# Kernel optimization log

Hardware: AMD Instinct MI355X
Metric: run time of the kernel (lower is better)

## Reference

```python
import jax, jax.numpy as jnp
import numpy as np

B, C, H, W = 8, 128, 256, 256
D = 64            # embed_dim
S = 32            # max_segments


def setup_inputs() -> dict:
    key = jax.random.key(0)
    ks = jax.random.split(key, 8)
    return {
        "segment_labels": jax.random.randint(ks[0], (B, 1, H, W), 0, S, dtype=jnp.int32),
        "features": jax.random.normal(ks[1], (B, C, H, W), jnp.float32),
        # 1x1 conv stack feat_proj: Conv2d(C->D), ReLU, Conv2d(D->D)
        "conv1_w": jax.random.normal(ks[2], (D, C), jnp.float32) * 0.05,
        "conv1_b": jnp.zeros((D,), jnp.float32),
        "conv2_w": jax.random.normal(ks[3], (D, D), jnp.float32) * 0.1,
        "conv2_b": jnp.zeros((D,), jnp.float32),
        # nn.Embedding(max_segments + 1, embed_dim)
        "embed_table": jax.random.normal(ks[4], (S + 1, D), jnp.float32) * 0.02,
        # nn.Linear(2*D, D): y = x @ W.T + b, W is (out, in)
        "out_w": jax.random.normal(ks[5], (D, 2 * D), jnp.float32) * 0.05,
        "out_b": jnp.zeros((D,), jnp.float32),
    }


def reference(segment_labels, features, conv1_w, conv1_b, conv2_w, conv2_b,
              embed_table, out_w, out_b):
    Bb, Cc, Hh, Ww = features.shape
    P = Hh * Ww
    Smax = embed_table.shape[0] - 1  # max_segments

    # feat_proj: two 1x1 convs == per-pixel GEMMs
    x = features.reshape(Bb, Cc, P)                                   # (B,C,P)
    h1 = jnp.maximum(jnp.einsum('oc,bcp->bpo', conv1_w, x) + conv1_b, 0.0)  # (B,P,D)
    feat = jnp.einsum('od,bpd->bpo', conv2_w, h1) + conv2_b           # (B,P,D)

    # Per-(batch, segment-id) masked mean via a single segment-sum pass.
    labels = segment_labels[:, 0].reshape(Bb, P)                       # (B,P) in [0,S)
    ids = (labels + Smax * jnp.arange(Bb, dtype=labels.dtype)[:, None]).reshape(-1)
    sums = jax.ops.segment_sum(feat.reshape(Bb * P, -1), ids,
                               num_segments=Bb * Smax).reshape(Bb, Smax, -1)
    counts = jax.ops.segment_sum(jnp.ones((Bb * P,), feat.dtype), ids,
                                 num_segments=Bb * Smax).reshape(Bb, Smax)
    pooled = sums / jnp.maximum(counts, 1.0)[..., None]                # (B,S,D) (zeros where absent)

    # type embedding for seg_id s (already in [0,S), clamp is a no-op but faithful)
    type_emb = embed_table[jnp.clip(jnp.arange(Smax), 0, Smax)]        # (S,D)
    combined = jnp.concatenate(
        [pooled, jnp.broadcast_to(type_emb, (Bb, Smax, type_emb.shape[-1]))], axis=-1)
    combined = jnp.einsum('oe,bse->bso', out_w, combined) + out_b      # (B,S,D)

    # torch.unique returns sorted present labels; compact present segments to the
    # front (rank order), pad rest with zeros.
    present = counts > 0                                               # (B,S)
    rank = jnp.cumsum(present.astype(jnp.int32), axis=1) - 1
    dst = jnp.where(present, rank, Smax)                               # Smax = dropped slot
    bidx = jnp.broadcast_to(jnp.arange(Bb)[:, None], (Bb, Smax))
    out = jnp.zeros_like(combined)
    out = out.at[bidx, dst].set(combined, mode='drop')
    return out
```

## Files before the change

### kernel.cpp

```cpp
#include <hip/hip_runtime.h>


#define B_ 8
#define C_ 128
#define P_ 65536
#define D_ 64
#define S_ 32
#define PXT 256
#define ROWPAD 260

typedef short bf16x8 __attribute__((ext_vector_type(8)));
typedef float f32x4  __attribute__((ext_vector_type(4)));

__device__ __forceinline__ short f2bf(float f) {
  union { float f; unsigned u; } v; v.f = f;
  unsigned r = v.u + 0x7fffu + ((v.u >> 16) & 1u);
  return (short)(r >> 16);
}

__global__ __launch_bounds__(256) void w1_to_bf16(const float* __restrict__ w1,
                                                  short* __restrict__ wbf) {
  int i = blockIdx.x * 256 + threadIdx.x;
  if (i < C_ * D_) wbf[i] = f2bf(w1[i]);
}

__device__ __forceinline__ void gload16(const float* g, const float* l) {
  __builtin_amdgcn_global_load_lds(
      (const __attribute__((address_space(1))) float*)g,
      (__attribute__((address_space(3))) float*)l, 16, 0, 0);
}

__global__ __launch_bounds__(256, 2) void proj_mfma(
    const int* __restrict__ labels, const float* __restrict__ feat,
    const short* __restrict__ wbf, const float* __restrict__ b1,
    float* __restrict__ gsum, int* __restrict__ gcnt)
{
  __shared__ __align__(16) float ring[4][16 * ROWPAD];
  __shared__ float s_acc[S_][68];
  __shared__ int   s_cnt[S_];

  const int tid  = threadIdx.x;
  const int wave = tid >> 6, l = tid & 63, m = l & 15, g = l >> 4;
  const int b    = blockIdx.y;
  const int px0  = blockIdx.x * PXT;

  for (int i = tid; i < S_ * 68; i += 256) ((float*)s_acc)[i] = 0.f;
  if (tid < S_) s_cnt[tid] = 0;

  bf16x8 bfr[4][4];
  #pragma unroll
  for (int nt = 0; nt < 4; ++nt)
    #pragma unroll
    for (int u = 0; u < 4; ++u)
      bfr[nt][u] = *(const bf16x8*)&wbf[(nt * 16 + m) * C_ + u * 32 + g * 8];
  float b1v[4];
  #pragma unroll
  for (int nt = 0; nt < 4; ++nt) b1v[nt] = b1[nt * 16 + m];

  const float* xb = feat + (size_t)b * C_ * P_ + px0;

#define STAGE(c_) do {                                                        \
    _Pragma("unroll") for (int i = 0; i < 4; ++i)                             \
      gload16(xb + (size_t)((c_) * 16 + wave * 4 + i) * P_ + l * 4,           \
              &ring[(c_) & 3][(wave * 4 + i) * ROWPAD]);                      \
  } while (0)

#define WAITV(n_) do {                                                        \
    asm volatile("s_waitcnt vmcnt(" #n_ ")" ::: "memory");                    \
    __builtin_amdgcn_sched_barrier(0);                                        \
  } while (0)

#define PAIR(u_) do {                                                         \
    _Pragma("unroll") for (int v = 0; v < 4; ++v) {                           \
      const int px = wave * 64 + v * 16 + m;                                  \
      const float* sl = &ring[(2 * (u_) + (g >> 1)) & 3]                      \
                             [((g & 1) * 8) * ROWPAD + px];                   \
      bf16x8 af;                                                              \
      _Pragma("unroll") for (int j = 0; j < 8; ++j)                           \
        af[j] = f2bf(sl[j * ROWPAD]);                                         \
      _Pragma("unroll") for (int nt = 0; nt < 4; ++nt)                        \
        acc[v][nt] = __builtin_amdgcn_mfma_f32_16x16x32_bf16(                 \
            af, bfr[nt][u_], acc[v][nt], 0, 0, 0);                            \
    }                                                                         \
  } while (0)

  STAGE(0); STAGE(1); STAGE(2); STAGE(3);

  f32x4 acc[4][4];
  #pragma unroll
  for (int v = 0; v < 4; ++v)
    #pragma unroll
    for (int nt = 0; nt < 4; ++nt) acc[v][nt] = (f32x4){0.f, 0.f, 0.f, 0.f};

  WAITV(8);
  __builtin_amdgcn_s_barrier();
  PAIR(0);
  __builtin_amdgcn_sched_barrier(0);
  __builtin_amdgcn_s_barrier();
  STAGE(4); STAGE(5);
  WAITV(8);
  __builtin_amdgcn_s_barrier();
  PAIR(1);
  __builtin_amdgcn_sched_barrier(0);
  __builtin_amdgcn_s_barrier();
  STAGE(6); STAGE(7);
  WAITV(8);
  __builtin_amdgcn_s_barrier();
  PAIR(2);
  __builtin_amdgcn_sched_barrier(0);
  WAITV(0);
  __builtin_amdgcn_s_barrier();
  PAIR(3);
  __builtin_amdgcn_sched_barrier(0);

#undef STAGE
#undef WAITV
#undef PAIR

  const int* lb = labels + (size_t)b * P_ + px0 + wave * 64;
  #pragma unroll
  for (int v = 0; v < 4; ++v) {
    const int4 lv = *(const int4*)&lb[v * 16 + g * 4];
    #pragma unroll
    for (int nt = 0; nt < 4; ++nt) {
      #pragma unroll
      for (int r = 0; r < 4; ++r) {
        const int lab = ((r & 2) ? ((r & 1) ? lv.w : lv.z)
                                 : ((r & 1) ? lv.y : lv.x)) & (S_ - 1);
        atomicAdd(&s_acc[lab][nt * 16 + m],
                  fmaxf(acc[v][nt][r] + b1v[nt], 0.f));
      }
    }
    if (m < 4) {
      const int lab = ((m & 2) ? ((m & 1) ? lv.w : lv.z)
                               : ((m & 1) ? lv.y : lv.x)) & (S_ - 1);
      atomicAdd(&s_cnt[lab], 1);
    }
  }

  __syncthreads();
  for (int i = tid; i < S_ * D_; i += 256)
    atomicAdd(&gsum[(size_t)b * S_ * D_ + i], s_acc[i >> 6][i & 63]);
  if (tid < S_) atomicAdd(&gcnt[b * S_ + tid], s_cnt[tid]);
}

__global__ __launch_bounds__(64) void seg_finalize2(
    const float* __restrict__ gsum, const int* __restrict__ gcnt,
    const float* __restrict__ w2, const float* __restrict__ b2,
    const float* __restrict__ emb, const float* __restrict__ wo,
    const float* __restrict__ bo, float* __restrict__ out)
{
  const int s = blockIdx.x, b = blockIdx.y, o = threadIdx.x;
  const int co = (o < S_) ? gcnt[b * S_ + o] : 0;
  const unsigned long long mask = __ballot(co > 0);
  const int cnt = gcnt[b * S_ + s];
  if (cnt <= 0) return;
  const int rank = __popcll(mask & ((1ull << s) - 1ull));

  __shared__ float s_mean[D_], s_pool[D_];
  s_mean[o] = gsum[((size_t)b * S_ + s) * D_ + o] * (1.f / (float)cnt);
  __syncthreads();
  float pooled = b2[o];
  #pragma unroll
  for (int d = 0; d < D_; ++d) pooled += w2[o * D_ + d] * s_mean[d];
  s_pool[o] = pooled;
  __syncthreads();
  float r = bo[o];
  #pragma unroll
  for (int e = 0; e < D_; ++e) r += wo[o * 2 * D_ + e] * s_pool[e];
  #pragma unroll
  for (int e = 0; e < D_; ++e) r += wo[o * 2 * D_ + D_ + e] * emb[s * D_ + e];
  out[((size_t)b * S_ + rank) * D_ + o] = r;
}

extern "C" void kernel_launch(void* const* d_in, const int* in_sizes, int n_in,
                              void* d_out, int out_size, void* d_ws, size_t ws_size,
                              hipStream_t stream) {
  const int*   labels = (const int*)  d_in[0];
  const float* feat   = (const float*)d_in[1];
  const float* w1     = (const float*)d_in[2];
  const float* b1     = (const float*)d_in[3];
  const float* w2     = (const float*)d_in[4];
  const float* b2     = (const float*)d_in[5];
  const float* emb    = (const float*)d_in[6];
  const float* wo     = (const float*)d_in[7];
  const float* bo     = (const float*)d_in[8];
  float* out = (float*)d_out;

  char* w = (char*)d_ws;
  float* gsum = (float*)w;   w += (size_t)B_ * S_ * D_ * 4;
  int*   gcnt = (int*)w;     w += (size_t)B_ * S_ * 4;
  short* wbf  = (short*)w;

  hipMemsetAsync(d_ws, 0, (size_t)B_ * S_ * D_ * 4 + (size_t)B_ * S_ * 4, stream);
  hipMemsetAsync(d_out, 0, (size_t)out_size * sizeof(float), stream);

  w1_to_bf16<<<(C_ * D_ + 255) / 256, 256, 0, stream>>>(w1, wbf);

  dim3 grid(P_ / PXT, B_);
  proj_mfma<<<grid, 256, 0, stream>>>(labels, feat, wbf, b1, gsum, gcnt);
  seg_finalize2<<<dim3(S_, B_), 64, 0, stream>>>(gsum, gcnt, w2, b2, emb, wo, bo, out);
}
```

Measured before the change: 233.0 us.

## Retile projection kernel to 1024-pixel blocks with 32x32 MFMA and LDS weights

Rewrites the projection kernel to use 512-thread blocks covering 1024 pixels each, with a 16-step ring pipeline over 8-channel slabs. It switches from 16x16x32 to 32x32x16 bf16 MFMA, stages the bf16 weights through padded LDS instead of per-thread registers, and remaps block ids so consecutive blocks land on different batches/XCDs. Fewer blocks mean fewer global atomic flushes of segment sums, but the larger LDS footprint and block size may reduce occupancy and latency hiding.

```diff
diff --git a/kernel.cpp b/kernel.cpp
--- a/kernel.cpp
+++ b/kernel.cpp
@@ -6,11 +6,12 @@
 #define P_ 65536
 #define D_ 64
 #define S_ 32
-#define PXT 256
-#define ROWPAD 260
+#define PXB 1024
+#define RP  1024
+#define WP  136
 
 typedef short bf16x8 __attribute__((ext_vector_type(8)));
-typedef float f32x4  __attribute__((ext_vector_type(4)));
+typedef float f32x16 __attribute__((ext_vector_type(16)));
 
 __device__ __forceinline__ short f2bf(float f) {
   union { float f; unsigned u; } v; v.f = f;
@@ -30,39 +31,37 @@
       (__attribute__((address_space(3))) float*)l, 16, 0, 0);
 }
 
-__global__ __launch_bounds__(256, 2) void proj_mfma(
+__global__ __launch_bounds__(512, 2) void proj_mfma(
     const int* __restrict__ labels, const float* __restrict__ feat,
     const short* __restrict__ wbf, const float* __restrict__ b1,
     float* __restrict__ gsum, int* __restrict__ gcnt)
 {
-  __shared__ __align__(16) float ring[4][16 * ROWPAD];
+  __shared__ __align__(16) float ring[4][8 * RP];
+  __shared__ __align__(16) short wlds[D_ * WP];
   __shared__ float s_acc[S_][68];
   __shared__ int   s_cnt[S_];
 
-  const int tid  = threadIdx.x;
-  const int wave = tid >> 6, l = tid & 63, m = l & 15, g = l >> 4;
-  const int b    = blockIdx.y;
-  const int px0  = blockIdx.x * PXT;
+  const int tid = threadIdx.x;
+  const int w = tid >> 6, l = tid & 63, n = l & 31, h = l >> 5;
+  const int bid = blockIdx.x;
+  const int wk  = (bid & 7) * 64 + (bid >> 3);
+  const int b   = wk >> 6;
+  const int px0 = (wk & 63) * PXB;
 
-  for (int i = tid; i < S_ * 68; i += 256) ((float*)s_acc)[i] = 0.f;
+  for (int i = tid; i < S_ * 68; i += 512) ((float*)s_acc)[i] = 0.f;
   if (tid < S_) s_cnt[tid] = 0;
-
-  bf16x8 bfr[4][4];
-  #pragma unroll
-  for (int nt = 0; nt < 4; ++nt)
-    #pragma unroll
-    for (int u = 0; u < 4; ++u)
-      bfr[nt][u] = *(const bf16x8*)&wbf[(nt * 16 + m) * C_ + u * 32 + g * 8];
-  float b1v[4];
-  #pragma unroll
-  for (int nt = 0; nt < 4; ++nt) b1v[nt] = b1[nt * 16 + m];
+  {
+    const int d = tid >> 3, c0 = (tid & 7) * 16;
+    *(bf16x8*)&wlds[d * WP + c0]     = *(const bf16x8*)&wbf[d * C_ + c0];
+    *(bf16x8*)&wlds[d * WP + c0 + 8] = *(const bf16x8*)&wbf[d * C_ + c0 + 8];
+  }
 
   const float* xb = feat + (size_t)b * C_ * P_ + px0;
 
-#define STAGE(c_) do {                                                        \
+#define STAGE(ci) do {                                                        \
     _Pragma("unroll") for (int i = 0; i < 4; ++i)                             \
-      gload16(xb + (size_t)((c_) * 16 + wave * 4 + i) * P_ + l * 4,           \
-              &ring[(c_) & 3][(wave * 4 + i) * ROWPAD]);                      \
+      gload16(xb + (size_t)((ci) * 8 + w) * P_ + i * 256 + l * 4,             \
+              &ring[(ci) & 3][w * RP + i * 256]);                             \
   } while (0)
 
 #define WAITV(n_) do {                                                        \
@@ -70,76 +69,67 @@
     __builtin_amdgcn_sched_barrier(0);                                        \
   } while (0)
 
-#define PAIR(u_) do {                                                         \
-    _Pragma("unroll") for (int v = 0; v < 4; ++v) {                           \
-      const int px = wave * 64 + v * 16 + m;                                  \
-      const float* sl = &ring[(2 * (u_) + (g >> 1)) & 3]                      \
-                             [((g & 1) * 8) * ROWPAD + px];                   \
-      bf16x8 af;                                                              \
-      _Pragma("unroll") for (int j = 0; j < 8; ++j)                           \
-        af[j] = f2bf(sl[j * ROWPAD]);                                         \
-      _Pragma("unroll") for (int nt = 0; nt < 4; ++nt)                        \
-        acc[v][nt] = __builtin_amdgcn_mfma_f32_16x16x32_bf16(                 \
-            af, bfr[nt][u_], acc[v][nt], 0, 0, 0);                            \
-    }                                                                         \
-  } while (0)
+  STAGE(0); STAGE(1); STAGE(2); STAGE(3);
+  asm volatile("s_waitcnt lgkmcnt(0)" ::: "memory");
+  __builtin_amdgcn_sched_barrier(0);
 
-  STAGE(0); STAGE(1); STAGE(2); STAGE(3);
-
-  f32x4 acc[4][4];
+  f32x16 acc[4][2];
   #pragma unroll
   for (int v = 0; v < 4; ++v)
     #pragma unroll
-    for (int nt = 0; nt < 4; ++nt) acc[v][nt] = (f32x4){0.f, 0.f, 0.f, 0.f};
+    for (int nt = 0; nt < 2; ++nt)
+      #pragma unroll
+      for (int e = 0; e < 16; ++e) acc[v][nt][e] = 0.f;
 
-  WAITV(8);
-  __builtin_amdgcn_s_barrier();
-  PAIR(0);
-  __builtin_amdgcn_sched_barrier(0);
-  __builtin_amdgcn_s_barrier();
-  STAGE(4); STAGE(5);
-  WAITV(8);
-  __builtin_amdgcn_s_barrier();
-  PAIR(1);
-  __builtin_amdgcn_sched_barrier(0);
-  __builtin_amdgcn_s_barrier();
-  STAGE(6); STAGE(7);
-  WAITV(8);
-  __builtin_amdgcn_s_barrier();
-  PAIR(2);
-  __builtin_amdgcn_sched_barrier(0);
-  WAITV(0);
-  __builtin_amdgcn_s_barrier();
-  PAIR(3);
-  __builtin_amdgcn_sched_barrier(0);
+  #pragma unroll
+  for (int ks = 0; ks < 8; ++ks) {
+    if (ks < 7) { WAITV(8); } else { WAITV(0); }
+    __builtin_amdgcn_s_barrier();
+    __builtin_amdgcn_sched_barrier(0);
 
+    const bf16x8 bw0 = *(const bf16x8*)&wlds[n * WP + ks * 16 + h * 8];
+    const bf16x8 bw1 = *(const bf16x8*)&wlds[(32 + n) * WP + ks * 16 + h * 8];
+    const float* rs = &ring[(2 * ks + h) & 3][0];
+    #pragma unroll
+    for (int v = 0; v < 4; ++v) {
+      bf16x8 af;
+      #pragma unroll
+      for (int j = 0; j < 8; ++j)
+        af[j] = f2bf(rs[j * RP + (w * 4 + v) * 32 + n]);
+      acc[v][0] = __builtin_amdgcn_mfma_f32_32x32x16_bf16(af, bw0, acc[v][0], 0, 0, 0);
+      acc[v][1] = __builtin_amdgcn_mfma_f32_32x32x16_bf16(af, bw1, acc[v][1], 0, 0, 0);
+    }
+    __builtin_amdgcn_sched_barrier(0);
+    __builtin_amdgcn_s_barrier();
+    __builtin_amdgcn_sched_barrier(0);
+    if (ks < 6) { STAGE(2 * ks + 4); STAGE(2 * ks + 5); }
+  }
 #undef STAGE
 #undef WAITV
-#undef PAIR
 
-  const int* lb = labels + (size_t)b * P_ + px0 + wave * 64;
+  const float b1v0 = b1[n];
+  const float b1v1 = b1[32 + n];
+  const int* lb = labels + (size_t)b * P_ + px0;
   #pragma unroll
   for (int v = 0; v < 4; ++v) {
-    const int4 lv = *(const int4*)&lb[v * 16 + g * 4];
+    const int tb = (w * 4 + v) * 32;
     #pragma unroll
-    for (int nt = 0; nt < 4; ++nt) {
+    for (int q = 0; q < 4; ++q) {
+      const int4 lv = *(const int4*)&lb[tb + q * 8 + h * 4];
       #pragma unroll
-      for (int r = 0; r < 4; ++r) {
-        const int lab = ((r & 2) ? ((r & 1) ? lv.w : lv.z)
-                                 : ((r & 1) ? lv.y : lv.x)) & (S_ - 1);
-        atomicAdd(&s_acc[lab][nt * 16 + m],
-                  fmaxf(acc[v][nt][r] + b1v[nt], 0.f));
+      for (int r2 = 0; r2 < 4; ++r2) {
+        const int lab = ((r2 & 2) ? ((r2 & 1) ? lv.w : lv.z)
+                                  : ((r2 & 1) ? lv.y : lv.x)) & (S_ - 1);
+        const int rg = q * 4 + r2;
+        atomicAdd(&s_acc[lab][n],      fmaxf(acc[v][0][rg] + b1v0, 0.f));
+        atomicAdd(&s_acc[lab][32 + n], fmaxf(acc[v][1][rg] + b1v1, 0.f));
+        if (n == 0) atomicAdd(&s_cnt[lab], 1);
       }
-    }
-    if (m < 4) {
-      const int lab = ((m & 2) ? ((m & 1) ? lv.w : lv.z)
-                               : ((m & 1) ? lv.y : lv.x)) & (S_ - 1);
-      atomicAdd(&s_cnt[lab], 1);
     }
   }
 
   __syncthreads();
-  for (int i = tid; i < S_ * D_; i += 256)
+  for (int i = tid; i < S_ * D_; i += 512)
     atomicAdd(&gsum[(size_t)b * S_ * D_ + i], s_acc[i >> 6][i & 63]);
   if (tid < S_) atomicAdd(&gcnt[b * S_ + tid], s_cnt[tid]);
 }
@@ -197,7 +187,6 @@
 
   w1_to_bf16<<<(C_ * D_ + 255) / 256, 256, 0, stream>>>(w1, wbf);
 
-  dim3 grid(P_ / PXT, B_);
-  proj_mfma<<<grid, 256, 0, stream>>>(labels, feat, wbf, b1, gsum, gcnt);
+  proj_mfma<<<(P_ / PXB) * B_, 512, 0, stream>>>(labels, feat, wbf, b1, gsum, gcnt);
   seg_finalize2<<<dim3(S_, B_), 64, 0, stream>>>(gsum, gcnt, w2, b2, emb, wo, bo, out);
 }
```

Result: faster. 223.9 us (-3.9%).
